# Kernel tuning notes

Hardware: AMD Instinct MI355X
Metric: run time of the kernel (lower is better)

Reference implementation:

```python
import jax, jax.numpy as jnp
import numpy as np

N = 4096          # nodes
IN_DIM = 256
OUT_DIM = 128
EDGE_DIM = 64
N_SAMPLE = 128
N_EDGES = 65536   # undirected edges (edge ids 1..N_EDGES; id 0 = no edge)
ALPHA = 0.2       # leaky-relu negative slope


def _glorot(key, shape):
    fan_in, fan_out = shape[0], shape[-1]
    scale = 1.414 * np.sqrt(2.0 / (fan_in + fan_out))
    return jax.random.normal(key, shape, jnp.float32) * scale


def setup_inputs() -> dict:
    rng = np.random.default_rng(0)
    # sample unique undirected edges (i < j); np.unique sorts lexicographically,
    # which matches torch's row-major e_index.nonzero() ordering, so assigning
    # sequential ids 1..n here makes edges == arange(1, n+1) in the update step.
    ii = rng.integers(0, N, size=3 * N_EDGES)
    jj = rng.integers(0, N, size=3 * N_EDGES)
    lo, hi = np.minimum(ii, jj), np.maximum(ii, jj)
    ok = lo < hi
    pairs = np.unique(np.stack([lo[ok], hi[ok]], axis=1), axis=0)[:N_EDGES]
    n = pairs.shape[0]
    ids = np.arange(1, n + 1, dtype=np.int32)
    e_index = np.zeros((N, N), np.int32)
    e_index[pairs[:, 0], pairs[:, 1]] = ids
    e_index[pairs[:, 1], pairs[:, 0]] = ids
    # per-node neighbor sampling with replacement (hoisted from torch forward)
    neigh = np.empty((N, N_SAMPLE), np.int32)
    for v in range(N):
        nz = np.nonzero(e_index[v])[0]
        neigh[v] = v if nz.size == 0 else rng.choice(nz, N_SAMPLE)

    key = jax.random.key(0)
    ks = jax.random.split(key, 8)
    return {
        "features": jax.random.normal(ks[0], (N, IN_DIM), jnp.float32),
        "e_index": jnp.asarray(e_index),
        "neigh": jnp.asarray(neigh),
        "to_update": jnp.asarray(pairs.astype(np.int32)),
        "emb": jax.random.normal(ks[1], (n + 1, EDGE_DIM), jnp.float32),
        "W": _glorot(ks[2], (IN_DIM, OUT_DIM)),
        "W2": _glorot(ks[3], (OUT_DIM, EDGE_DIM)),
        "W3": _glorot(ks[4], (EDGE_DIM, EDGE_DIM)),
        "B": _glorot(ks[5], (1, EDGE_DIM)),
        "a": _glorot(ks[6], (2 * OUT_DIM + EDGE_DIM, 1)),
    }


def reference(features, e_index, neigh, to_update, emb, W, W2, W3, B, a):
    x = features @ W                                        # [N, OUT]
    xn = x[neigh]                                           # [N, S, OUT] gather
    eid = jnp.take_along_axis(e_index, neigh, axis=1)       # [N, S] edge ids
    en = emb[eid]                                           # [N, S, ED] gather
    a_input = jnp.concatenate(
        [jnp.broadcast_to(x[:, None, :], xn.shape), xn, en], axis=2
    )                                                       # [N, S, 2*OUT+ED]
    e = jax.nn.leaky_relu((a_input @ a)[..., 0], ALPHA)     # [N, S]
    att = jax.nn.softmax(e, axis=1)                         # dropout = id (eval)
    h_prime = jnp.einsum('ns,nsd->nd', att, xn)             # [N, OUT]
    output = jax.nn.elu(h_prime + x)
    # edge update: (output[i] + output[j]) @ W2 == matmul(output[pair], W2).sum(1)
    edges = e_index[to_update[:, 0], to_update[:, 1]]       # == 1..n
    v_input = (output[to_update[:, 0]] + output[to_update[:, 1]]) @ W2
    e_input = emb[edges] @ W3
    a_in2 = jnp.concatenate([B, e_input + v_input + B], axis=0)  # [n+1, ED]
    emb_new = jax.nn.relu(a_in2 * emb)
    return output, emb_new
```

## Files before the change

### kernel.cpp

```cpp
#include <hip/hip_runtime.h>
#include <hip/hip_bf16.h>

#define N_NODES 4096
#define IN_DIM  256
#define OUT_DIM 128
#define EDGE_DIM 64
#define N_SAMPLE 128

__device__ __forceinline__ float wsum64(float v) {
#pragma unroll
  for (int off = 32; off; off >>= 1) v += __shfl_xor(v, off, 64);
  return v;
}
__device__ __forceinline__ float sum16(float v) {
#pragma unroll
  for (int off = 1; off < 16; off <<= 1) v += __shfl_xor(v, off, 64);
  return v;
}
__device__ __forceinline__ float bfu(ushort u) {
  return __uint_as_float((unsigned int)u << 16);
}

__global__ void __launch_bounds__(256) k1_kernel(const float* __restrict__ feat,
                                                 const float* __restrict__ W,
                                                 const float* __restrict__ emb,
                                                 const int* __restrict__ eidx,
                                                 const int* __restrict__ neigh,
                                                 const int* __restrict__ tu,
                                                 const float* __restrict__ a,
                                                 const float* __restrict__ W3,
                                                 const float* __restrict__ Bv,
                                                 ushort* __restrict__ xh,
                                                 float* __restrict__ s1,
                                                 float* __restrict__ s2,
                                                 float* __restrict__ s3,
                                                 int* __restrict__ eid_vs,
                                                 float* __restrict__ Z,
                                                 int n, int rows) {
  const int t   = threadIdx.x;
  const int bid = blockIdx.x;
  const int v0  = bid * 4;
  const int k0z = bid * 64;
  __shared__ float U[4352];
  __shared__ float redA[8], redB[8];
  __shared__ int   tusS[128];
  __shared__ int   eidS[64];

  if (t < 128) tusS[t] = (2 * k0z + t < 2 * n) ? tu[2 * k0z + t] : 0;
  int uq[2];
#pragma unroll
  for (int q = 0; q < 2; ++q) {
    const int idx = t + 256 * q, r = idx >> 7, s = idx & 127;
    uq[q] = neigh[(v0 + r) * N_SAMPLE + s];
  }
  reinterpret_cast<float4*>(U)[t] =
      reinterpret_cast<const float4*>(&feat[v0 * IN_DIM])[t];
  __syncthreads();

  int eq[2];
#pragma unroll
  for (int q = 0; q < 2; ++q) {
    const int idx = t + 256 * q, r = idx >> 7;
    eq[q] = eidx[(v0 + r) * N_NODES + uq[q]];
  }
  if (t < 64) {
    const int ke = k0z + t;
    eidS[t] = (ke < n) ? eidx[tusS[2 * t] * N_NODES + tusS[2 * t + 1]] : 0;
  }

  const int h = t >> 7, c = t & 127;
  {
    float acc4[4] = {0.f, 0.f, 0.f, 0.f};
    const int kb = h * 128;
    for (int k = kb; k < kb + 128; k += 4) {
      const float w0 = W[(k + 0) * OUT_DIM + c];
      const float w1 = W[(k + 1) * OUT_DIM + c];
      const float w2 = W[(k + 2) * OUT_DIM + c];
      const float w3 = W[(k + 3) * OUT_DIM + c];
#pragma unroll
      for (int r = 0; r < 4; ++r) {
        const float4 fv = *reinterpret_cast<const float4*>(&U[r * 256 + k]);
        acc4[r] += fv.x * w0 + fv.y * w1 + fv.z * w2 + fv.w * w3;
      }
    }
#pragma unroll
    for (int r = 0; r < 4; ++r) U[1024 + (h * 4 + r) * 128 + c] = acc4[r];
  }
  __syncthreads();

  if (t < 128) {
    const float a1t = a[t], a2t = a[OUT_DIM + t];
    const int wv = t >> 6;
#pragma unroll
    for (int r = 0; r < 4; ++r) {
      const float xv = U[1024 + r * 128 + t] + U[1024 + (4 + r) * 128 + t];
      unsigned int ub = __float_as_uint(xv);
      ub += 0x7FFFu + ((ub >> 16) & 1u);
      xh[(v0 + r) * OUT_DIM + t] = (ushort)(ub >> 16);
      const float q1 = wsum64(xv * a1t);
      const float q2 = wsum64(xv * a2t);
      if ((t & 63) == 0) { redA[wv * 4 + r] = q1; redB[wv * 4 + r] = q2; }
    }
  }
#pragma unroll
  for (int q = 0; q < 2; ++q) {
    const int idx = t + 256 * q, r = idx >> 7, s = idx & 127;
    eid_vs[(v0 + r) * N_SAMPLE + s] = eq[q];
  }
  __syncthreads();
  if (t < 4) {
    s1[v0 + t] = redA[t] + redA[4 + t];
    s2[v0 + t] = redB[t] + redB[4 + t];
  }

  {
    const int wv = t >> 6, l = t & 63;
    const int gw = bid * 4 + wv;
    const int sub = l >> 4, q16 = l & 15;
    const float4 a3q = *reinterpret_cast<const float4*>(&a[2 * OUT_DIM + q16 * 4]);
    for (int r0 = gw * 4; r0 < rows; r0 += 16384) {
      const int r = r0 + sub;
      float v = 0.f;
      if (r < rows) {
        const float4 e4 = *reinterpret_cast<const float4*>(&emb[r * EDGE_DIM + q16 * 4]);
        v = e4.x * a3q.x + e4.y * a3q.y + e4.z * a3q.z + e4.w * a3q.w;
      }
      v = sum16(v);
      if (q16 == 0 && r < rows) s3[r] = v;
    }
  }
  __syncthreads();

  if (k0z < n) {
    const int e = t >> 2, q = t & 3;
    const int id = eidS[e];
#pragma unroll
    for (int kk = 0; kk < 16; kk += 4) {
      const int k = q * 16 + kk;
      *reinterpret_cast<float4*>(&U[e * 68 + k]) =
          *reinterpret_cast<const float4*>(&emb[id * EDGE_DIM + k]);
    }
  }
  __syncthreads();

  if (k0z < n) {
    const int e0 = (t >> 4) * 4;
    const int c0 = (t & 15) * 4;
    const float4 b4 = *reinterpret_cast<const float4*>(&Bv[c0]);
    float4 acc[4];
#pragma unroll
    for (int m = 0; m < 4; ++m) acc[m] = b4;
#pragma unroll 4
    for (int k = 0; k < EDGE_DIM; k += 4) {
      float4 a4[4];
#pragma unroll
      for (int m = 0; m < 4; ++m)
        a4[m] = *reinterpret_cast<const float4*>(&U[(e0 + m) * 68 + k]);
#pragma unroll
      for (int kk = 0; kk < 4; ++kk) {
        const float4 wv = *reinterpret_cast<const float4*>(&W3[(k + kk) * EDGE_DIM + c0]);
#pragma unroll
        for (int m = 0; m < 4; ++m) {
          const float av = reinterpret_cast<const float*>(&a4[m])[kk];
          acc[m].x += av * wv.x; acc[m].y += av * wv.y;
          acc[m].z += av * wv.z; acc[m].w += av * wv.w;
        }
      }
    }
#pragma unroll
    for (int m = 0; m < 4; ++m) {
      const int ke = k0z + e0 + m;
      if (ke < n)
        *reinterpret_cast<float4*>(&Z[ke * EDGE_DIM + c0]) = acc[m];
    }
  }
}

__global__ void __launch_bounds__(256, 4) k2_attn_y_kernel(const ushort* __restrict__ xh,
                                                           const float* __restrict__ s1,
                                                           const float* __restrict__ s2,
                                                           const float* __restrict__ s3,
                                                           const int* __restrict__ neigh,
                                                           const int* __restrict__ eid_vs,
                                                           const float* __restrict__ W2,
                                                           float* __restrict__ out,
                                                           float* __restrict__ Y) {
  const int v = blockIdx.x;
  const int t = threadIdx.x;
  const int w = t >> 6, l = t & 63;
  __shared__ float attC[N_SAMPLE];
  __shared__ float redC[2];
  __shared__ float4 hpC[8][32];
  __shared__ float orow[OUT_DIM];
  __shared__ float partY[4][EDGE_DIM];

  const int half = l >> 5, cq = l & 31;
  const int s0 = w * 32;
  ushort4 xr[16];
#pragma unroll
  for (int it = 0; it < 16; ++it) {
    const int u = neigh[v * N_SAMPLE + s0 + 2 * it + half];
    xr[it] = *reinterpret_cast<const ushort4*>(&xh[u * OUT_DIM + cq * 4]);
  }

  if (t < N_SAMPLE) {
    const int u   = neigh[v * N_SAMPLE + t];
    const int eid = eid_vs[v * N_SAMPLE + t];
    float e = s1[v] + s2[u] + s3[eid];
    e = e > 0.f ? e : 0.2f * e;
    const float p = __expf(e);
    attC[t] = p;
    const float s = wsum64(p);
    if (l == 0) redC[w] = s;
  }
  __syncthreads();
  const float inv = 1.0f / (redC[0] + redC[1]);

  {
    float4 h4 = make_float4(0.f, 0.f, 0.f, 0.f);
#pragma unroll
    for (int it = 0; it < 16; ++it) {
      const float av = attC[s0 + 2 * it + half];
      h4.x += av * bfu(xr[it].x);
      h4.y += av * bfu(xr[it].y);
      h4.z += av * bfu(xr[it].z);
      h4.w += av * bfu(xr[it].w);
    }
    hpC[w * 2 + half][cq] = h4;
  }
  __syncthreads();

  if (t < 32) {
    float4 H = make_float4(0.f, 0.f, 0.f, 0.f);
#pragma unroll
    for (int p = 0; p < 8; ++p) {
      const float4 v4 = hpC[p][t];
      H.x += v4.x; H.y += v4.y; H.z += v4.z; H.w += v4.w;
    }
    const ushort4 xs = *reinterpret_cast<const ushort4*>(&xh[v * OUT_DIM + t * 4]);
    float o0 = H.x * inv + bfu(xs.x), o1 = H.y * inv + bfu(xs.y);
    float o2 = H.z * inv + bfu(xs.z), o3 = H.w * inv + bfu(xs.w);
    o0 = o0 > 0.f ? o0 : expm1f(o0);
    o1 = o1 > 0.f ? o1 : expm1f(o1);
    o2 = o2 > 0.f ? o2 : expm1f(o2);
    o3 = o3 > 0.f ? o3 : expm1f(o3);
    const float4 r = make_float4(o0, o1, o2, o3);
    *reinterpret_cast<float4*>(&out[v * OUT_DIM + t * 4]) = r;
    *reinterpret_cast<float4*>(&orow[t * 4]) = r;
  }
  __syncthreads();

  {
    const int c = t & 63, ks = t >> 6;
    float acc = 0.f;
#pragma unroll 8
    for (int k = ks * 32; k < ks * 32 + 32; ++k)
      acc += orow[k] * W2[k * EDGE_DIM + c];
    partY[ks][c] = acc;
  }
  __syncthreads();
  if (t < EDGE_DIM)
    Y[v * EDGE_DIM + t] = partY[0][t] + partY[1][t] + partY[2][t] + partY[3][t];
}

__global__ void __launch_bounds__(256) k3_kernel(const float* __restrict__ Z,
                                                 const float* __restrict__ Y,
                                                 const float* __restrict__ emb,
                                                 const int* __restrict__ tu,
                                                 const float* __restrict__ Bv,
                                                 float* __restrict__ emb_new, int n) {
  const int t  = threadIdx.x;
  const int k0 = blockIdx.x * 64;
  __shared__ int tus[128];
  if (t < 128) tus[t] = (2 * k0 + t < 2 * n) ? tu[2 * k0 + t] : 0;
  __syncthreads();

  const int e0 = (t >> 4) * 4;
  const int c0 = (t & 15) * 4;
#pragma unroll
  for (int m = 0; m < 4; ++m) {
    const int ke = k0 + e0 + m;
    if (ke < n) {
      const int i = tus[2 * (e0 + m)], j = tus[2 * (e0 + m) + 1];
      const float4 z4 = *reinterpret_cast<const float4*>(&Z[ke * EDGE_DIM + c0]);
      const float4 yi = *reinterpret_cast<const float4*>(&Y[i * EDGE_DIM + c0]);
      const float4 yj = *reinterpret_cast<const float4*>(&Y[j * EDGE_DIM + c0]);
      const float4 ek = *reinterpret_cast<const float4*>(&emb[(ke + 1) * EDGE_DIM + c0]);
      float4 r;
      r.x = fmaxf((z4.x + yi.x + yj.x) * ek.x, 0.f);
      r.y = fmaxf((z4.y + yi.y + yj.y) * ek.y, 0.f);
      r.z = fmaxf((z4.z + yi.z + yj.z) * ek.z, 0.f);
      r.w = fmaxf((z4.w + yi.w + yj.w) * ek.w, 0.f);
      *reinterpret_cast<float4*>(&emb_new[(ke + 1) * EDGE_DIM + c0]) = r;
    }
  }
  if (blockIdx.x == 0 && t < 16) {
    const int cc = t * 4;
    const float4 b0 = *reinterpret_cast<const float4*>(&Bv[cc]);
    const float4 e0v = *reinterpret_cast<const float4*>(&emb[cc]);
    float4 r;
    r.x = fmaxf(b0.x * e0v.x, 0.f);
    r.y = fmaxf(b0.y * e0v.y, 0.f);
    r.z = fmaxf(b0.z * e0v.z, 0.f);
    r.w = fmaxf(b0.w * e0v.w, 0.f);
    *reinterpret_cast<float4*>(&emb_new[cc]) = r;
  }
}

extern "C" void kernel_launch(void* const* d_in, const int* in_sizes, int n_in,
                              void* d_out, int out_size, void* d_ws, size_t ws_size,
                              hipStream_t stream) {
  const float* feat  = (const float*)d_in[0];
  const int*   eidx  = (const int*)d_in[1];
  const int*   neigh = (const int*)d_in[2];
  const int*   tu    = (const int*)d_in[3];
  const float* emb   = (const float*)d_in[4];
  const float* W     = (const float*)d_in[5];
  const float* W2    = (const float*)d_in[6];
  const float* W3    = (const float*)d_in[7];
  const float* Bv    = (const float*)d_in[8];
  const float* a     = (const float*)d_in[9];
  const int n    = in_sizes[3] / 2;
  const int rows = in_sizes[4] / EDGE_DIM;

  float* ws = (float*)d_ws;
  float* s1     = ws + 524288;
  float* s2     = ws + 528384;
  float* s3     = ws + 532480;
  float* Y      = ws + 598032;
  ushort* xh    = (ushort*)(ws + 860176);
  int*  eid_vs  = (int*)(ws + 1122320);
  float* Z      = ws + 1646608;

  float* out_nodes = (float*)d_out;
  float* emb_new   = out_nodes + N_NODES * OUT_DIM;

  hipLaunchKernelGGL(k1_kernel, dim3(N_NODES / 4), dim3(256), 0, stream,
                     feat, W, emb, eidx, neigh, tu, a, W3, Bv,
                     xh, s1, s2, s3, eid_vs, Z, n, rows);
  hipLaunchKernelGGL(k2_attn_y_kernel, dim3(N_NODES), dim3(256), 0, stream,
                     xh, s1, s2, s3, neigh, eid_vs, W2, out_nodes, Y);
  hipLaunchKernelGGL(k3_kernel, dim3((n + 63) / 64), dim3(256), 0, stream,
                     Z, Y, emb, tu, Bv, emb_new, n);
}
```

Baseline: 172.7 us.

## Use bf16 MFMA for feature projection and W3 edge matmul in k1

Adds a small kernel that converts and transposes W and W3 to bf16, then rewrites the two GEMMs in k1 (features@W and emb@W3) to use 16x16x32 bf16 MFMA instructions instead of scalar FP32 FMAs. The node part now processes 16 nodes per block on only the first 256 blocks, while all 1024 blocks still handle edges. This lowers ALU work in k1 but costs an extra launch and reduces the precision of the x and Z projections to bf16 inputs.

```diff
diff --git a/kernel.cpp b/kernel.cpp
--- a/kernel.cpp
+++ b/kernel.cpp
@@ -7,6 +7,9 @@
 #define EDGE_DIM 64
 #define N_SAMPLE 128
 
+typedef __attribute__((ext_vector_type(8))) short bf16x8;
+typedef __attribute__((ext_vector_type(4))) float f32x4;
+
 __device__ __forceinline__ float wsum64(float v) {
 #pragma unroll
   for (int off = 32; off; off >>= 1) v += __shfl_xor(v, off, 64);
@@ -20,15 +23,35 @@
 __device__ __forceinline__ float bfu(ushort u) {
   return __uint_as_float((unsigned int)u << 16);
 }
+__device__ __forceinline__ ushort f2b(float x) {
+  unsigned int u = __float_as_uint(x);
+  u += 0x7FFFu + ((u >> 16) & 1u);
+  return (ushort)(u >> 16);
+}
+
+__global__ void __launch_bounds__(256) k0_convert(const float* __restrict__ W,
+                                                  const float* __restrict__ W3,
+                                                  ushort* __restrict__ Wt,
+                                                  ushort* __restrict__ W3t) {
+  const int id = blockIdx.x * 256 + threadIdx.x;
+  if (id < IN_DIM * OUT_DIM) {
+    const int k = id >> 7, c = id & 127;
+    Wt[c * IN_DIM + k] = f2b(W[id]);
+  } else if (id < IN_DIM * OUT_DIM + EDGE_DIM * EDGE_DIM) {
+    const int j = id - IN_DIM * OUT_DIM;
+    const int k = j >> 6, c = j & 63;
+    W3t[c * EDGE_DIM + k] = f2b(W3[j]);
+  }
+}
 
 __global__ void __launch_bounds__(256) k1_kernel(const float* __restrict__ feat,
-                                                 const float* __restrict__ W,
+                                                 const ushort* __restrict__ Wt,
                                                  const float* __restrict__ emb,
                                                  const int* __restrict__ eidx,
                                                  const int* __restrict__ neigh,
                                                  const int* __restrict__ tu,
                                                  const float* __restrict__ a,
-                                                 const float* __restrict__ W3,
+                                                 const ushort* __restrict__ W3t,
                                                  const float* __restrict__ Bv,
                                                  ushort* __restrict__ xh,
                                                  float* __restrict__ s1,
@@ -39,83 +62,99 @@
                                                  int n, int rows) {
   const int t   = threadIdx.x;
   const int bid = blockIdx.x;
-  const int v0  = bid * 4;
+  const int v0  = bid * 16;
   const int k0z = bid * 64;
-  __shared__ float U[4352];
-  __shared__ float redA[8], redB[8];
-  __shared__ int   tusS[128];
-  __shared__ int   eidS[64];
-
-  if (t < 128) tusS[t] = (2 * k0z + t < 2 * n) ? tu[2 * k0z + t] : 0;
-  int uq[2];
-#pragma unroll
-  for (int q = 0; q < 2; ++q) {
-    const int idx = t + 256 * q, r = idx >> 7, s = idx & 127;
-    uq[q] = neigh[(v0 + r) * N_SAMPLE + s];
-  }
-  reinterpret_cast<float4*>(U)[t] =
-      reinterpret_cast<const float4*>(&feat[v0 * IN_DIM])[t];
-  __syncthreads();
-
-  int eq[2];
-#pragma unroll
-  for (int q = 0; q < 2; ++q) {
-    const int idx = t + 256 * q, r = idx >> 7;
-    eq[q] = eidx[(v0 + r) * N_NODES + uq[q]];
-  }
-  if (t < 64) {
-    const int ke = k0z + t;
-    eidS[t] = (ke < n) ? eidx[tusS[2 * t] * N_NODES + tusS[2 * t + 1]] : 0;
-  }
-
-  const int h = t >> 7, c = t & 127;
+  const bool doA = (bid < 256);
+
+  __shared__ __align__(16) char smem[17408];
+  ushort* Abf   = reinterpret_cast<ushort*>(smem);
+  float*  xtile = reinterpret_cast<float*>(smem + 8448);
+  ushort* Ain   = reinterpret_cast<ushort*>(smem);
+  __shared__ float redA[32], redB[32];
+  __shared__ int tus[128];
+  __shared__ int eidS[64];
+
+  const int w = t >> 6, l = t & 63, lr = l & 15, lk = l >> 4;
+
+  if (t < 128) tus[t] = (2 * k0z + t < 2 * n) ? tu[2 * k0z + t] : 0;
+  int uq[8];
+  if (doA) {
+#pragma unroll
+    for (int q = 0; q < 8; ++q) {
+      const int idx = t + 256 * q, r = idx >> 7, s = idx & 127;
+      uq[q] = neigh[(v0 + r) * N_SAMPLE + s];
+    }
+    const int row = t >> 4, ch = t & 15;
+    const float4* src = reinterpret_cast<const float4*>(&feat[(v0 + row) * IN_DIM + ch * 16]);
+    const float4 f0 = src[0], f1 = src[1], f2 = src[2], f3 = src[3];
+    bf16x8 p0, p1;
+    p0[0]=(short)f2b(f0.x); p0[1]=(short)f2b(f0.y); p0[2]=(short)f2b(f0.z); p0[3]=(short)f2b(f0.w);
+    p0[4]=(short)f2b(f1.x); p0[5]=(short)f2b(f1.y); p0[6]=(short)f2b(f1.z); p0[7]=(short)f2b(f1.w);
+    p1[0]=(short)f2b(f2.x); p1[1]=(short)f2b(f2.y); p1[2]=(short)f2b(f2.z); p1[3]=(short)f2b(f2.w);
+    p1[4]=(short)f2b(f3.x); p1[5]=(short)f2b(f3.y); p1[6]=(short)f2b(f3.z); p1[7]=(short)f2b(f3.w);
+    *reinterpret_cast<bf16x8*>(&Abf[row * 264 + ch * 16])     = p0;
+    *reinterpret_cast<bf16x8*>(&Abf[row * 264 + ch * 16 + 8]) = p1;
+  }
+  __syncthreads();
+
+  if (t < 64)
+    eidS[t] = (k0z + t < n) ? eidx[tus[2 * t] * N_NODES + tus[2 * t + 1]] : 0;
+  int eq[8];
+  if (doA) {
+#pragma unroll
+    for (int q = 0; q < 8; ++q) {
+      const int idx = t + 256 * q, r = idx >> 7;
+      eq[q] = eidx[(v0 + r) * N_NODES + uq[q]];
+    }
+  }
+
+  if (doA) {
+    f32x4 acc0 = {0.f, 0.f, 0.f, 0.f}, acc1 = {0.f, 0.f, 0.f, 0.f};
+    const ushort* b0p = Wt + (w * 32 + lr) * IN_DIM;
+    const ushort* b1p = Wt + (w * 32 + 16 + lr) * IN_DIM;
+#pragma unroll
+    for (int ks = 0; ks < 8; ++ks) {
+      const bf16x8 af = *reinterpret_cast<const bf16x8*>(&Abf[lr * 264 + ks * 32 + lk * 8]);
+      const bf16x8 b0 = *reinterpret_cast<const bf16x8*>(b0p + ks * 32 + lk * 8);
+      const bf16x8 b1 = *reinterpret_cast<const bf16x8*>(b1p + ks * 32 + lk * 8);
+      acc0 = __builtin_amdgcn_mfma_f32_16x16x32_bf16(af, b0, acc0, 0, 0, 0);
+      acc1 = __builtin_amdgcn_mfma_f32_16x16x32_bf16(af, b1, acc1, 0, 0, 0);
+    }
+#pragma unroll
+    for (int r = 0; r < 4; ++r) {
+      xtile[(lk * 4 + r) * 132 + w * 32 + lr]      = acc0[r];
+      xtile[(lk * 4 + r) * 132 + w * 32 + 16 + lr] = acc1[r];
+    }
+  }
+  __syncthreads();
+
+  if (doA) {
+#pragma unroll
+    for (int q = 0; q < 8; ++q) {
+      const int idx = t + 256 * q, r = idx >> 7, s = idx & 127;
+      eid_vs[(v0 + r) * N_SAMPLE + s] = eq[q];
+    }
+    if (t < 128) {
+      const float a1t = a[t], a2t = a[OUT_DIM + t];
+      const int wv = t >> 6;
+#pragma unroll
+      for (int r = 0; r < 16; ++r) {
+        const float xv = xtile[r * 132 + t];
+        xh[(v0 + r) * OUT_DIM + t] = f2b(xv);
+        const float q1 = wsum64(xv * a1t);
+        const float q2 = wsum64(xv * a2t);
+        if ((t & 63) == 0) { redA[wv * 16 + r] = q1; redB[wv * 16 + r] = q2; }
+      }
+    }
+  }
+  __syncthreads();
+  if (doA && t < 16) {
+    s1[v0 + t] = redA[t] + redA[16 + t];
+    s2[v0 + t] = redB[t] + redB[16 + t];
+  }
+
   {
-    float acc4[4] = {0.f, 0.f, 0.f, 0.f};
-    const int kb = h * 128;
-    for (int k = kb; k < kb + 128; k += 4) {
-      const float w0 = W[(k + 0) * OUT_DIM + c];
-      const float w1 = W[(k + 1) * OUT_DIM + c];
-      const float w2 = W[(k + 2) * OUT_DIM + c];
-      const float w3 = W[(k + 3) * OUT_DIM + c];
-#pragma unroll
-      for (int r = 0; r < 4; ++r) {
-        const float4 fv = *reinterpret_cast<const float4*>(&U[r * 256 + k]);
-        acc4[r] += fv.x * w0 + fv.y * w1 + fv.z * w2 + fv.w * w3;
-      }
-    }
-#pragma unroll
-    for (int r = 0; r < 4; ++r) U[1024 + (h * 4 + r) * 128 + c] = acc4[r];
-  }
-  __syncthreads();
-
-  if (t < 128) {
-    const float a1t = a[t], a2t = a[OUT_DIM + t];
-    const int wv = t >> 6;
-#pragma unroll
-    for (int r = 0; r < 4; ++r) {
-      const float xv = U[1024 + r * 128 + t] + U[1024 + (4 + r) * 128 + t];
-      unsigned int ub = __float_as_uint(xv);
-      ub += 0x7FFFu + ((ub >> 16) & 1u);
-      xh[(v0 + r) * OUT_DIM + t] = (ushort)(ub >> 16);
-      const float q1 = wsum64(xv * a1t);
-      const float q2 = wsum64(xv * a2t);
-      if ((t & 63) == 0) { redA[wv * 4 + r] = q1; redB[wv * 4 + r] = q2; }
-    }
-  }
-#pragma unroll
-  for (int q = 0; q < 2; ++q) {
-    const int idx = t + 256 * q, r = idx >> 7, s = idx & 127;
-    eid_vs[(v0 + r) * N_SAMPLE + s] = eq[q];
-  }
-  __syncthreads();
-  if (t < 4) {
-    s1[v0 + t] = redA[t] + redA[4 + t];
-    s2[v0 + t] = redB[t] + redB[4 + t];
-  }
-
-  {
-    const int wv = t >> 6, l = t & 63;
-    const int gw = bid * 4 + wv;
+    const int gw = bid * 4 + w;
     const int sub = l >> 4, q16 = l & 15;
     const float4 a3q = *reinterpret_cast<const float4*>(&a[2 * OUT_DIM + q16 * 4]);
     for (int r0 = gw * 4; r0 < rows; r0 += 16384) {
@@ -132,46 +171,46 @@
   __syncthreads();
 
   if (k0z < n) {
-    const int e = t >> 2, q = t & 3;
+    const int e = t >> 2, q4 = t & 3;
     const int id = eidS[e];
-#pragma unroll
-    for (int kk = 0; kk < 16; kk += 4) {
-      const int k = q * 16 + kk;
-      *reinterpret_cast<float4*>(&U[e * 68 + k]) =
-          *reinterpret_cast<const float4*>(&emb[id * EDGE_DIM + k]);
-    }
+    const float4* src = reinterpret_cast<const float4*>(&emb[id * EDGE_DIM + q4 * 16]);
+    const float4 f0 = src[0], f1 = src[1], f2 = src[2], f3 = src[3];
+    bf16x8 p0, p1;
+    p0[0]=(short)f2b(f0.x); p0[1]=(short)f2b(f0.y); p0[2]=(short)f2b(f0.z); p0[3]=(short)f2b(f0.w);
+    p0[4]=(short)f2b(f1.x); p0[5]=(short)f2b(f1.y); p0[6]=(short)f2b(f1.z); p0[7]=(short)f2b(f1.w);
+    p1[0]=(short)f2b(f2.x); p1[1]=(short)f2b(f2.y); p1[2]=(short)f2b(f2.z); p1[3]=(short)f2b(f2.w);
+    p1[4]=(short)f2b(f3.x); p1[5]=(short)f2b(f3.y); p1[6]=(short)f2b(f3.z); p1[7]=(short)f2b(f3.w);
+    *reinterpret_cast<bf16x8*>(&Ain[e * 72 + q4 * 16])     = p0;
+    *reinterpret_cast<bf16x8*>(&Ain[e * 72 + q4 * 16 + 8]) = p1;
   }
   __syncthreads();
 
   if (k0z < n) {
-    const int e0 = (t >> 4) * 4;
-    const int c0 = (t & 15) * 4;
-    const float4 b4 = *reinterpret_cast<const float4*>(&Bv[c0]);
-    float4 acc[4];
-#pragma unroll
-    for (int m = 0; m < 4; ++m) acc[m] = b4;
-#pragma unroll 4
-    for (int k = 0; k < EDGE_DIM; k += 4) {
-      float4 a4[4];
-#pragma unroll
-      for (int m = 0; m < 4; ++m)
-        a4[m] = *reinterpret_cast<const float4*>(&U[(e0 + m) * 68 + k]);
-#pragma unroll
-      for (int kk = 0; kk < 4; ++kk) {
-        const float4 wv = *reinterpret_cast<const float4*>(&W3[(k + kk) * EDGE_DIM + c0]);
-#pragma unroll
-        for (int m = 0; m < 4; ++m) {
-          const float av = reinterpret_cast<const float*>(&a4[m])[kk];
-          acc[m].x += av * wv.x; acc[m].y += av * wv.y;
-          acc[m].z += av * wv.z; acc[m].w += av * wv.w;
-        }
+    f32x4 za0 = {0.f,0.f,0.f,0.f}, za1 = {0.f,0.f,0.f,0.f};
+    f32x4 za2 = {0.f,0.f,0.f,0.f}, za3 = {0.f,0.f,0.f,0.f};
+    const ushort* ap = Ain + (w * 16 + lr) * 72;
+#pragma unroll
+    for (int ks = 0; ks < 2; ++ks) {
+      const bf16x8 af = *reinterpret_cast<const bf16x8*>(ap + ks * 32 + lk * 8);
+      const bf16x8 b0 = *reinterpret_cast<const bf16x8*>(W3t + (0 * 16 + lr) * EDGE_DIM + ks * 32 + lk * 8);
+      const bf16x8 b1 = *reinterpret_cast<const bf16x8*>(W3t + (1 * 16 + lr) * EDGE_DIM + ks * 32 + lk * 8);
+      const bf16x8 b2 = *reinterpret_cast<const bf16x8*>(W3t + (2 * 16 + lr) * EDGE_DIM + ks * 32 + lk * 8);
+      const bf16x8 b3 = *reinterpret_cast<const bf16x8*>(W3t + (3 * 16 + lr) * EDGE_DIM + ks * 32 + lk * 8);
+      za0 = __builtin_amdgcn_mfma_f32_16x16x32_bf16(af, b0, za0, 0, 0, 0);
+      za1 = __builtin_amdgcn_mfma_f32_16x16x32_bf16(af, b1, za1, 0, 0, 0);
+      za2 = __builtin_amdgcn_mfma_f32_16x16x32_bf16(af, b2, za2, 0, 0, 0);
+      za3 = __builtin_amdgcn_mfma_f32_16x16x32_bf16(af, b3, za3, 0, 0, 0);
+    }
+    const float bv0 = Bv[lr], bv1 = Bv[16 + lr], bv2 = Bv[32 + lr], bv3 = Bv[48 + lr];
+#pragma unroll
+    for (int r = 0; r < 4; ++r) {
+      const int ke = k0z + w * 16 + lk * 4 + r;
+      if (ke < n) {
+        Z[ke * EDGE_DIM + lr]      = za0[r] + bv0;
+        Z[ke * EDGE_DIM + 16 + lr] = za1[r] + bv1;
+        Z[ke * EDGE_DIM + 32 + lr] = za2[r] + bv2;
+        Z[ke * EDGE_DIM + 48 + lr] = za3[r] + bv3;
       }
-    }
-#pragma unroll
-    for (int m = 0; m < 4; ++m) {
-      const int ke = k0z + e0 + m;
-      if (ke < n)
-        *reinterpret_cast<float4*>(&Z[ke * EDGE_DIM + c0]) = acc[m];
     }
   }
 }
@@ -331,12 +370,15 @@
   ushort* xh    = (ushort*)(ws + 860176);
   int*  eid_vs  = (int*)(ws + 1122320);
   float* Z      = ws + 1646608;
+  ushort* Wt    = (ushort*)(ws + 5840912);
+  ushort* W3t   = (ushort*)(ws + 5857296);
 
   float* out_nodes = (float*)d_out;
   float* emb_new   = out_nodes + N_NODES * OUT_DIM;
 
-  hipLaunchKernelGGL(k1_kernel, dim3(N_NODES / 4), dim3(256), 0, stream,
-                     feat, W, emb, eidx, neigh, tu, a, W3, Bv,
+  hipLaunchKernelGGL(k0_convert, dim3(144), dim3(256), 0, stream, W, W3, Wt, W3t);
+  hipLaunchKernelGGL(k1_kernel, dim3(1024), dim3(256), 0, stream,
+                     feat, Wt, emb, eidx, neigh, tu, a, W3t, Bv,
                      xh, s1, s2, s3, eid_vs, Z, n, rows);
   hipLaunchKernelGGL(k2_attn_y_kernel, dim3(N_NODES), dim3(256), 0, stream,
                      xh, s1, s2, s3, neigh, eid_vs, W2, out_nodes, Y);
```

Result: faster. 165.3 us (-4.3%).
